# Performance work log

Measured on AMD Instinct MI355X. Metric: run time of the kernel, lower is better.

## Reference

```python
import jax, jax.numpy as jnp
import numpy as np

DEPTH = 2
DIM = 192
HEADS = 6
MLP_RATIO = 4

def _layernorm(x, g, b):
    mu = jnp.mean(x, -1, keepdims=True)
    var = jnp.var(x, -1, keepdims=True)
    return (x - mu) * jax.lax.rsqrt(var + 1e-5) * g + b

def _scanline_order(pos, w):
    # default space-filling curve of space_filling_cluster: horizontal scanlines
    # with alternating direction in each row (boustrophedon order)
    ix = jnp.floor(pos[..., 0]).astype(jnp.int32)
    iy = jnp.floor(pos[..., 1]).astype(jnp.int32)
    key = iy * w + jnp.where(iy % 2 == 1, w - 1 - ix, ix)
    order_idx = jnp.argsort(key, axis=1)      # rank -> token idx (b, n)
    inv_idx = jnp.argsort(order_idx, axis=1)  # token idx -> rank (b, n)
    return order_idx, inv_idx

def setup_inputs():
    key = jax.random.key(0)
    ks = jax.random.split(key, 8)
    b, h, w, m = 4, 128, 128, 64
    n = h * w
    d = DIM
    dff = MLP_RATIO * d
    s = 0.02
    x = jax.random.normal(ks[0], (b, n, d), jnp.float32)
    # token positions: the full h x w grid, randomly permuted per batch element
    ys, xs = jnp.meshgrid(jnp.arange(h), jnp.arange(w), indexing='ij')
    grid = jnp.stack([xs.reshape(-1), ys.reshape(-1)], -1).astype(jnp.float32)
    perm = jax.vmap(lambda kk: jax.random.permutation(kk, n))(jax.random.split(ks[1], b))
    pos = grid[perm]  # (b, n, 2)
    return {
        'x': x, 'pos': pos,
        'ln1_g': jnp.ones((DEPTH, d)), 'ln1_b': jnp.zeros((DEPTH, d)),
        'w_qkv': jax.random.normal(ks[2], (DEPTH, d, 3 * d), jnp.float32) * s,
        'b_qkv': jnp.zeros((DEPTH, 3 * d)),
        'w_proj': jax.random.normal(ks[3], (DEPTH, d, d), jnp.float32) * s,
        'b_proj': jnp.zeros((DEPTH, d)),
        'ln2_g': jnp.ones((DEPTH, d)), 'ln2_b': jnp.zeros((DEPTH, d)),
        'w_fc1': jax.random.normal(ks[4], (DEPTH, d, dff), jnp.float32) * s,
        'b_fc1': jnp.zeros((DEPTH, dff)),
        'w_fc2': jax.random.normal(ks[5], (DEPTH, dff, d), jnp.float32) * s,
        'b_fc2': jnp.zeros((DEPTH, d)),
        'h': h, 'w': w, 'm': m,
    }

def reference(x, pos, ln1_g, ln1_b, w_qkv, b_qkv, w_proj, b_proj,
              ln2_g, ln2_b, w_fc1, b_fc1, w_fc2, b_fc2, h, w, m):
    b, n, d = x.shape
    dh = d // HEADS
    scale = dh ** -0.5
    kc = n // m  # number of clusters (n chosen divisible by m -> all-ones cluster_mask)
    # clustering is computed under no_grad in the original -> stop_gradient
    order_idx, inv_idx = _scanline_order(jax.lax.stop_gradient(pos), w)
    for i in range(DEPTH):
        # --- cluster attention ---
        xn = _layernorm(x, ln1_g[i], ln1_b[i])
        qkv = xn @ w_qkv[i] + b_qkv[i]                                  # (b, n, 3d)
        qkv = jnp.take_along_axis(qkv, order_idx[..., None], axis=1)    # gather into curve order
        qkv = qkv.reshape(b, kc, m, 3, HEADS, dh)
        q = jnp.transpose(qkv[:, :, :, 0], (0, 1, 3, 2, 4))             # (b, kc, H, m, dh)
        kk = jnp.transpose(qkv[:, :, :, 1], (0, 1, 3, 2, 4))
        v = jnp.transpose(qkv[:, :, :, 2], (0, 1, 3, 2, 4))
        att = jax.nn.softmax(jnp.einsum('bkhqd,bkhpd->bkhqp', q, kk) * scale, axis=-1)
        o = jnp.einsum('bkhqp,bkhpd->bkhqd', att, v)
        o = jnp.transpose(o, (0, 1, 3, 2, 4)).reshape(b, n, d)
        o = jnp.take_along_axis(o, inv_idx[..., None], axis=1)          # scatter back to token order
        x = x + o @ w_proj[i] + b_proj[i]
        # --- MLP ---
        yn = _layernorm(x, ln2_g[i], ln2_b[i])
        x = x + jax.nn.gelu(yn @ w_fc1[i] + b_fc1[i]) @ w_fc2[i] + b_fc2[i]
    return x
```

## Files before the change

### kernel.cpp

```cpp
#include <hip/hip_runtime.h>
#include <hip/hip_bf16.h>

typedef __hip_bfloat16 bf16;
typedef __attribute__((ext_vector_type(8))) short short8;
typedef __attribute__((ext_vector_type(4))) short s16x4;
typedef __attribute__((ext_vector_type(4))) float f32x4;

#define B_   4
#define N_   16384
#define D_   192
#define H6   6
#define DH   32
#define MCL  64
#define KC   256
#define DFF  768
#define GW   128
#define MTOK (B_ * N_)
#define XST  196

__device__ __forceinline__ bf16 f2b(float x) { return __float2bfloat16(x); }
__device__ __forceinline__ short f2bbits(float x) {
    bf16 h = __float2bfloat16(x); return *(short*)&h;
}

__global__ void zero_out_kernel(float* __restrict__ out, size_t n) {
    size_t i = blockIdx.x * (size_t)blockDim.x + threadIdx.x;
    if (i < n) out[i] = 0.f;
}

__global__ void build_idx(const float* __restrict__ pos, int* __restrict__ order) {
    int tid = blockIdx.x * blockDim.x + threadIdx.x;
    if (tid >= B_ * N_) return;
    int b = tid / N_;
    int ix = (int)floorf(pos[(size_t)tid * 2 + 0]);
    int iy = (int)floorf(pos[(size_t)tid * 2 + 1]);
    int key = iy * GW + ((iy & 1) ? (GW - 1 - ix) : ix);
    key = (int)(((unsigned)key) & (N_ - 1));
    order[(size_t)b * N_ + key] = tid % N_;
}

__global__ void wprep_all(const float* __restrict__ wq, const float* __restrict__ wp,
                          const float* __restrict__ wf1, const float* __restrict__ wf2,
                          bf16* __restrict__ out) {
    int tid = blockIdx.x * blockDim.x + threadIdx.x;
    if (tid >= 2 * 442368) return;
    int l = tid / 442368, r = tid % 442368;
    const float* src; bf16* dst; int K, Nn, e;
    if (r < 110592)      { src = wq  + (size_t)l * 110592; dst = out + (size_t)l * 442368;          K = 192; Nn = 576; e = r; }
    else if (r < 147456) { src = wp  + (size_t)l * 36864;  dst = out + (size_t)l * 442368 + 110592; K = 192; Nn = 192; e = r - 110592; }
    else if (r < 294912) { src = wf1 + (size_t)l * 147456; dst = out + (size_t)l * 442368 + 147456; K = 192; Nn = 768; e = r - 147456; }
    else                 { src = wf2 + (size_t)l * 147456; dst = out + (size_t)l * 442368 + 294912; K = 768; Nn = 192; e = r - 294912; }
    int k = e / Nn, n = e % Nn;
    int idx = ((n >> 4) * (K >> 5) + (k >> 5)) * 512 + (((k >> 3) & 3) * 16 + (n & 15)) * 8 + (k & 7);
    dst[idx] = f2b(src[e]);
}

template<bool GELU>
__global__ __launch_bounds__(256, 4) void gemm_lnk192(
    const float* __restrict__ Ain, const float* __restrict__ lng, const float* __restrict__ lnb,
    const bf16* __restrict__ Wf, const float* __restrict__ bias,
    bf16* __restrict__ Cout, int Nn) {
    __shared__ short Asl[4 * 6 * 512];
    int tid = threadIdx.x;
    int bm = blockIdx.x;
    int w = tid >> 6, lane = tid & 63;
    {
        int r = tid >> 2, qq = tid & 3;
        const float* xr = Ain + ((size_t)(bm * 64) + r) * 192 + qq * 48;
        float4 va[12];
        float s = 0.f, ss = 0.f;
        #pragma unroll
        for (int j = 0; j < 12; j++) {
            va[j] = ((const float4*)xr)[j];
            s  += va[j].x + va[j].y + va[j].z + va[j].w;
            ss += va[j].x * va[j].x + va[j].y * va[j].y + va[j].z * va[j].z + va[j].w * va[j].w;
        }
        s  += __shfl_xor(s, 1);  s  += __shfl_xor(s, 2);
        ss += __shfl_xor(ss, 1); ss += __shfl_xor(ss, 2);
        float mean = s * (1.f / 192.f);
        float var  = ss * (1.f / 192.f) - mean * mean;
        float rs   = rsqrtf(var + 1e-5f);
        const float4* gg = (const float4*)(lng + qq * 48);
        const float4* bb = (const float4*)(lnb + qq * 48);
        #pragma unroll
        for (int j = 0; j < 6; j++) {
            float4 g0 = gg[2 * j], g1 = gg[2 * j + 1], b0 = bb[2 * j], b1 = bb[2 * j + 1];
            float4 x0 = va[2 * j], x1 = va[2 * j + 1];
            short8 o;
            o[0] = f2bbits((x0.x - mean) * rs * g0.x + b0.x);
            o[1] = f2bbits((x0.y - mean) * rs * g0.y + b0.y);
            o[2] = f2bbits((x0.z - mean) * rs * g0.z + b0.z);
            o[3] = f2bbits((x0.w - mean) * rs * g0.w + b0.w);
            o[4] = f2bbits((x1.x - mean) * rs * g1.x + b1.x);
            o[5] = f2bbits((x1.y - mean) * rs * g1.y + b1.y);
            o[6] = f2bbits((x1.z - mean) * rs * g1.z + b1.z);
            o[7] = f2bbits((x1.w - mean) * rs * g1.w + b1.w);
            int k0 = qq * 48 + j * 8;
            int kt = k0 >> 5, qd = (k0 >> 3) & 3;
            *(short8*)&Asl[((r >> 4) * 6 + kt) * 512 + (qd * 16 + (r & 15)) * 8] = o;
        }
    }
    __syncthreads();
    short8 af[6];
    #pragma unroll
    for (int kt = 0; kt < 6; kt++)
        af[kt] = *(short8*)&Asl[(w * 6 + kt) * 512 + lane * 8];
    int quad = lane >> 4, l16 = lane & 15;
    int ntiles = Nn >> 4;
    for (int nt = 0; nt < ntiles; nt++) {
        const short* bp = (const short*)Wf + ((size_t)nt * 6) * 512 + lane * 8;
        f32x4 acc = {};
        #pragma unroll
        for (int kt = 0; kt < 6; kt++) {
            short8 b = *(const short8*)(bp + kt * 512);
            acc = __builtin_amdgcn_mfma_f32_16x16x32_bf16(af[kt], b, acc, 0, 0, 0);
        }
        int col = nt * 16 + l16;
        float bv = bias[col];
        int row0 = bm * 64 + w * 16 + quad * 4;
        #pragma unroll
        for (int rr = 0; rr < 4; rr++) {
            float v = acc[rr] + bv;
            if (GELU) {
                float inner = 0.7978845608028654f * (v + 0.044715f * v * v * v);
                inner = fminf(fmaxf(inner, -12.f), 12.f);
                float e = __expf(2.f * inner);
                v = 0.5f * v * (1.f + (e - 1.f) / (e + 1.f));
            }
            Cout[(size_t)(row0 + rr) * Nn + col] = f2b(v);
        }
    }
}

__global__ __launch_bounds__(256) void pm_fused(
    const bf16* __restrict__ Anob,
    const bf16* __restrict__ Wpf, const float* __restrict__ bp_,
    const float* __restrict__ Rsrc,
    const float* __restrict__ lng, const float* __restrict__ lnb,
    const bf16* __restrict__ W1f, const float* __restrict__ b1,
    const bf16* __restrict__ W2f, const float* __restrict__ b2,
    float* __restrict__ Rdst) {
    __shared__ float Xl[64 * XST];
    __shared__ short Bsl[4 * 6 * 512];
    short* Asl = (short*)Xl;
    int tid = threadIdx.x;
    int bm = blockIdx.x;
    int w = tid >> 6, lane = tid & 63;
    int quad = lane >> 4, l16 = lane & 15;
    {
        int r = tid >> 2, qq = tid & 3;
        const short* ar = (const short*)Anob + ((size_t)(bm * 64) + r) * 192 + qq * 48;
        #pragma unroll
        for (int j = 0; j < 6; j++) {
            short8 v = *(const short8*)(ar + j * 8);
            int k0 = qq * 48 + j * 8;
            int kt = k0 >> 5, qd = (k0 >> 3) & 3;
            *(short8*)&Asl[((r >> 4) * 6 + kt) * 512 + (qd * 16 + (r & 15)) * 8] = v;
        }
    }
    __syncthreads();
    short8 afp[6];
    #pragma unroll
    for (int kt = 0; kt < 6; kt++)
        afp[kt] = *(short8*)&Asl[(w * 6 + kt) * 512 + lane * 8];
    f32x4 acc[12];
    #pragma unroll
    for (int nt = 0; nt < 12; nt++) {
        const short* bp = (const short*)Wpf + ((size_t)nt * 6) * 512 + lane * 8;
        f32x4 a = {};
        #pragma unroll
        for (int kt = 0; kt < 6; kt++) {
            short8 b = *(const short8*)(bp + kt * 512);
            a = __builtin_amdgcn_mfma_f32_16x16x32_bf16(afp[kt], b, a, 0, 0, 0);
        }
        acc[nt] = a;
    }
    __syncthreads();
    #pragma unroll
    for (int nt = 0; nt < 12; nt++) {
        int col = nt * 16 + l16;
        float bv = bp_[col];
        int lr0 = w * 16 + quad * 4;
        #pragma unroll
        for (int rr = 0; rr < 4; rr++) {
            float rv = Rsrc[(size_t)(bm * 64 + lr0 + rr) * 192 + col];
            Xl[(lr0 + rr) * XST + col] = acc[nt][rr] + bv + rv;
        }
    }
    __syncthreads();
    {
        int r = tid >> 2, qq = tid & 3;
        const float* xr = &Xl[r * XST + qq * 48];
        float4 va[12];
        float s = 0.f, ss = 0.f;
        #pragma unroll
        for (int j = 0; j < 12; j++) {
            va[j] = ((const float4*)xr)[j];
            s  += va[j].x + va[j].y + va[j].z + va[j].w;
            ss += va[j].x * va[j].x + va[j].y * va[j].y + va[j].z * va[j].z + va[j].w * va[j].w;
        }
        s  += __shfl_xor(s, 1);  s  += __shfl_xor(s, 2);
        ss += __shfl_xor(ss, 1); ss += __shfl_xor(ss, 2);
        float mean = s * (1.f / 192.f);
        float var  = ss * (1.f / 192.f) - mean * mean;
        float rs   = rsqrtf(var + 1e-5f);
        const float4* gg = (const float4*)(lng + qq * 48);
        const float4* bb = (const float4*)(lnb + qq * 48);
        #pragma unroll
        for (int j = 0; j < 6; j++) {
            float4 g0 = gg[2 * j], g1 = gg[2 * j + 1], b0 = bb[2 * j], b1v = bb[2 * j + 1];
            float4 x0 = va[2 * j], x1 = va[2 * j + 1];
            short8 o;
            o[0] = f2bbits((x0.x - mean) * rs * g0.x + b0.x);
            o[1] = f2bbits((x0.y - mean) * rs * g0.y + b0.y);
            o[2] = f2bbits((x0.z - mean) * rs * g0.z + b0.z);
            o[3] = f2bbits((x0.w - mean) * rs * g0.w + b0.w);
            o[4] = f2bbits((x1.x - mean) * rs * g1.x + b1v.x);
            o[5] = f2bbits((x1.y - mean) * rs * g1.y + b1v.y);
            o[6] = f2bbits((x1.z - mean) * rs * g1.z + b1v.z);
            o[7] = f2bbits((x1.w - mean) * rs * g1.w + b1v.w);
            int k0 = qq * 48 + j * 8;
            int kt = k0 >> 5, qd = (k0 >> 3) & 3;
            *(short8*)&Bsl[((r >> 4) * 6 + kt) * 512 + (qd * 16 + (r & 15)) * 8] = o;
        }
    }
    __syncthreads();
    short8 af[4][6];
    #pragma unroll
    for (int mt = 0; mt < 4; mt++)
        #pragma unroll
        for (int kt = 0; kt < 6; kt++)
            af[mt][kt] = *(short8*)&Bsl[(mt * 6 + kt) * 512 + lane * 8];
    f32x4 acc2[3][4] = {};
    for (int qtr = 0; qtr < 4; qtr++) {
        __syncthreads();
        #pragma unroll
        for (int j = 0; j < 3; j++) {
            int nth = w * 3 + j;
            int ntg = qtr * 12 + nth;
            const short* bp = (const short*)W1f + ((size_t)ntg * 6) * 512 + lane * 8;
            short8 bfr[6];
            #pragma unroll
            for (int kt = 0; kt < 6; kt++) bfr[kt] = *(const short8*)(bp + kt * 512);
            #pragma unroll
            for (int mt = 0; mt < 4; mt++) {
                f32x4 a = {};
                #pragma unroll
                for (int kt = 0; kt < 6; kt++)
                    a = __builtin_amdgcn_mfma_f32_16x16x32_bf16(bfr[kt], af[mt][kt], a, 0, 0, 0);
                int colb = ntg * 16 + quad * 4;
                s16x4 o;
                #pragma unroll
                for (int rr = 0; rr < 4; rr++) {
                    float u = a[rr] + b1[colb + rr];
                    float inner = 0.7978845608028654f * (u + 0.044715f * u * u * u);
                    inner = fminf(fmaxf(inner, -12.f), 12.f);
                    float e = __expf(2.f * inner);
                    o[rr] = f2bbits(0.5f * u * (1.f + (e - 1.f) / (e + 1.f)));
                }
                *(s16x4*)&Bsl[(mt * 6 + (nth >> 1)) * 512
                              + (((nth & 1) * 2 + (quad >> 1)) * 16 + l16) * 8 + (quad & 1) * 4] = o;
            }
        }
        __syncthreads();
        #pragma unroll
        for (int kt = 0; kt < 6; kt++) {
            short8 afh[4];
            #pragma unroll
            for (int mt = 0; mt < 4; mt++)
                afh[mt] = *(short8*)&Bsl[(mt * 6 + kt) * 512 + lane * 8];
            #pragma unroll
            for (int j = 0; j < 3; j++) {
                int nt = w * 3 + j;
                const short* bp = (const short*)W2f + ((size_t)nt * 24 + qtr * 6 + kt) * 512 + lane * 8;
                short8 b = *(const short8*)bp;
                #pragma unroll
                for (int mt = 0; mt < 4; mt++)
                    acc2[j][mt] = __builtin_amdgcn_mfma_f32_16x16x32_bf16(afh[mt], b, acc2[j][mt], 0, 0, 0);
            }
        }
    }
    #pragma unroll
    for (int j = 0; j < 3; j++) {
        int col = (w * 3 + j) * 16 + l16;
        float bv = b2[col];
        #pragma unroll
        for (int mt = 0; mt < 4; mt++) {
            int lr0 = mt * 16 + quad * 4;
            #pragma unroll
            for (int rr = 0; rr < 4; rr++) {
                size_t idx = (size_t)(bm * 64 + lr0 + rr) * 192 + col;
                Rdst[idx] = acc2[j][mt][rr] + bv + Xl[(lr0 + rr) * XST + col];
            }
        }
    }
}

#define PST 72
#define VST 72
#define OST 40
__global__ __launch_bounds__(64) void attn_mfma(const bf16* __restrict__ qkv,
                                                const int* __restrict__ order,
                                                bf16* __restrict__ outb) {
    __shared__ short vT[32 * VST];
    __shared__ short Pl[64 * PST];
    const float scale = 0.17677669529663687f;
    int h = blockIdx.x, c = blockIdx.y, b = blockIdx.z;
    int lane = threadIdx.x;
    int l16 = lane & 15, quad = lane >> 4;
    int t = (int)(((unsigned)order[(size_t)b * N_ + c * MCL + lane]) & (N_ - 1));
    const short* qb = (const short*)qkv + (size_t)b * N_ * 576;
    {
        const short* vp = qb + (size_t)t * 576 + 384 + h * 32;
        short8 v[4];
        #pragma unroll
        for (int i = 0; i < 4; i++) v[i] = *(const short8*)(vp + i * 8);
        #pragma unroll
        for (int i = 0; i < 4; i++)
            #pragma unroll
            for (int e = 0; e < 8; e++)
                vT[(i * 8 + e) * VST + lane] = v[i][e];
    }
    short8 aq[4], bk[4];
    #pragma unroll
    for (int i = 0; i < 4; i++) {
        int tr = __shfl(t, i * 16 + l16);
        const short* rp = qb + (size_t)tr * 576 + h * 32 + quad * 8;
        aq[i] = *(const short8*)rp;
        bk[i] = *(const short8*)(rp + 192);
    }
    f32x4 S[4][4];
    #pragma unroll
    for (int mt = 0; mt < 4; mt++)
        #pragma unroll
        for (int nt = 0; nt < 4; nt++) {
            f32x4 z = {};
            S[mt][nt] = __builtin_amdgcn_mfma_f32_16x16x32_bf16(aq[mt], bk[nt], z, 0, 0, 0);
        }
    __syncthreads();
    #pragma unroll
    for (int mt = 0; mt < 4; mt++)
        #pragma unroll
        for (int r = 0; r < 4; r++) {
            float e0, e1, e2, e3, s;
            float v0 = S[mt][0][r] * scale, v1 = S[mt][1][r] * scale;
            float v2 = S[mt][2][r] * scale, v3 = S[mt][3][r] * scale;
            e0 = __expf(fminf(fmaxf(v0, -30.f), 30.f));
            e1 = __expf(fminf(fmaxf(v1, -30.f), 30.f));
            e2 = __expf(fminf(fmaxf(v2, -30.f), 30.f));
            e3 = __expf(fminf(fmaxf(v3, -30.f), 30.f));
            s = e0 + e1 + e2 + e3;
            s += __shfl_xor(s, 1); s += __shfl_xor(s, 2);
            s += __shfl_xor(s, 4); s += __shfl_xor(s, 8);
            float inv = 1.f / s;
            int row = mt * 16 + quad * 4 + r;
            Pl[row * PST +  0 + l16] = f2bbits(e0 * inv);
            Pl[row * PST + 16 + l16] = f2bbits(e1 * inv);
            Pl[row * PST + 32 + l16] = f2bbits(e2 * inv);
            Pl[row * PST + 48 + l16] = f2bbits(e3 * inv);
        }
    __syncthreads();
    short8 ap[4][2], bv[2][2];
    #pragma unroll
    for (int mt = 0; mt < 4; mt++)
        #pragma unroll
        for (int kt = 0; kt < 2; kt++)
            ap[mt][kt] = *(const short8*)&Pl[(mt * 16 + l16) * PST + kt * 32 + quad * 8];
    #pragma unroll
    for (int nt = 0; nt < 2; nt++)
        #pragma unroll
        for (int kt = 0; kt < 2; kt++)
            bv[nt][kt] = *(const short8*)&vT[(nt * 16 + l16) * VST + kt * 32 + quad * 8];
    f32x4 O[4][2] = {};
    #pragma unroll
    for (int mt = 0; mt < 4; mt++)
        #pragma unroll
        for (int nt = 0; nt < 2; nt++)
            #pragma unroll
            for (int kt = 0; kt < 2; kt++)
                O[mt][nt] = __builtin_amdgcn_mfma_f32_16x16x32_bf16(ap[mt][kt], bv[nt][kt], O[mt][nt], 0, 0, 0);
    __syncthreads();
    short* Ol = Pl;
    #pragma unroll
    for (int mt = 0; mt < 4; mt++) {
        int row = mt * 16 + quad * 4;
        #pragma unroll
        for (int nt = 0; nt < 2; nt++)
            #pragma unroll
            for (int rr = 0; rr < 4; rr++)
                Ol[(row + rr) * OST + nt * 16 + l16] = f2bbits(O[mt][nt][rr]);
    }
    __syncthreads();
    short* op = (short*)outb + ((size_t)b * N_ + t) * 192 + h * 32;
    #pragma unroll
    for (int j = 0; j < 4; j++)
        *(short8*)(op + j * 8) = *(const short8*)&Ol[lane * OST + j * 8];
}

extern "C" void kernel_launch(void* const* d_in, const int* in_sizes, int n_in,
                              void* d_out, int out_size, void* d_ws, size_t ws_size,
                              hipStream_t stream) {
    const float* x_in   = (const float*)d_in[0];
    const float* pos    = (const float*)d_in[1];
    const float* ln1_g  = (const float*)d_in[2];
    const float* ln1_b  = (const float*)d_in[3];
    const float* w_qkv  = (const float*)d_in[4];
    const float* b_qkv  = (const float*)d_in[5];
    const float* w_proj = (const float*)d_in[6];
    const float* b_proj = (const float*)d_in[7];
    const float* ln2_g  = (const float*)d_in[8];
    const float* ln2_b  = (const float*)d_in[9];
    const float* w_fc1  = (const float*)d_in[10];
    const float* b_fc1  = (const float*)d_in[11];
    const float* w_fc2  = (const float*)d_in[12];
    const float* b_fc2  = (const float*)d_in[13];

    size_t sz_x     = (size_t)MTOK * D_ * 4;
    size_t sz_xnob  = (size_t)MTOK * D_ * 2;
    size_t sz_cbuf  = (size_t)MTOK * DFF * 2;
    size_t sz_order = (size_t)B_ * N_ * 4;
    size_t sz_wbuf  = (size_t)2 * 442368 * 2;
    size_t need = sz_x + sz_xnob + sz_cbuf + sz_order + sz_wbuf;
    if (ws_size < need) {
        zero_out_kernel<<<(out_size + 255) / 256, 256, 0, stream>>>((float*)d_out, (size_t)out_size);
        return;
    }
    char* ws = (char*)d_ws;
    float* x_f32 = (float*)ws;  ws += sz_x;
    bf16*  xnob  = (bf16*)ws;   ws += sz_xnob;
    bf16*  cbuf  = (bf16*)ws;   ws += sz_cbuf;
    int*   order = (int*)ws;    ws += sz_order;
    bf16*  wbuf  = (bf16*)ws;   ws += sz_wbuf;

    bf16* wq[2]; bf16* wp[2]; bf16* wf1[2]; bf16* wf2[2];
    for (int l = 0; l < 2; ++l) {
        bf16* p = wbuf + (size_t)l * 442368;
        wq[l]  = p;
        wp[l]  = p + 110592;
        wf1[l] = p + 147456;
        wf2[l] = p + 294912;
    }
    wprep_all<<<(2 * 442368 + 255) / 256, 256, 0, stream>>>(w_qkv, w_proj, w_fc1, w_fc2, wbuf);
    build_idx<<<(B_ * N_ + 255) / 256, 256, 0, stream>>>(pos, order);

    for (int l = 0; l < 2; ++l) {
        const float* xsrc = (l == 0) ? x_in : x_f32;
        float* rdst = (l == 1) ? (float*)d_out : x_f32;
        gemm_lnk192<false><<<MTOK / 64, 256, 0, stream>>>(
            xsrc, ln1_g + l * D_, ln1_b + l * D_, wq[l], b_qkv + l * 576, cbuf, 576);
        attn_mfma<<<dim3(H6, KC, B_), 64, 0, stream>>>(cbuf, order, xnob);
        pm_fused<<<MTOK / 64, 256, 0, stream>>>(
            xnob, wp[l], b_proj + l * 192, xsrc,
            ln2_g + l * D_, ln2_b + l * D_,
            wf1[l], b_fc1 + l * 768, wf2[l], b_fc2 + l * 192,
            rdst);
    }
}
```

Baseline: 510.5 us.

## Fuse LayerNorm, QKV projection and cluster attention into one kernel

Replaces the separate LN+QKV GEMM kernel and the per-head attention kernel with one kernel that runs per cluster and batch element. The kernel gathers the cluster's token rows in curve order, applies LayerNorm, and computes Q, K and V into shared memory with one wave per head. Each wave then runs softmax attention on its own head and writes the output back to token order. This removes the full qkv intermediate buffer and its global write and reread. In exchange it needs a large shared-memory footprint and 384-thread blocks, which may limit how many blocks fit on each CU.

New measurement: 440.3 us. 1.16x faster.

```diff
diff --git a/kernel.cpp b/kernel.cpp
--- a/kernel.cpp
+++ b/kernel.cpp
@@ -17,6 +17,8 @@
 #define GW   128
 #define MTOK (B_ * N_)
 #define XST  196
+#define PST  72
+#define OST  40
 
 __device__ __forceinline__ bf16 f2b(float x) { return __float2bfloat16(x); }
 __device__ __forceinline__ short f2bbits(float x) {
@@ -55,18 +57,26 @@
     dst[idx] = f2b(src[e]);
 }
 
-template<bool GELU>
-__global__ __launch_bounds__(256, 4) void gemm_lnk192(
-    const float* __restrict__ Ain, const float* __restrict__ lng, const float* __restrict__ lnb,
-    const bf16* __restrict__ Wf, const float* __restrict__ bias,
-    bf16* __restrict__ Cout, int Nn) {
+__global__ __launch_bounds__(384) void qa_fused(
+    const float* __restrict__ xsrc, const int* __restrict__ order,
+    const float* __restrict__ lng, const float* __restrict__ lnb,
+    const bf16* __restrict__ Wqf, const float* __restrict__ bq,
+    bf16* __restrict__ outb) {
     __shared__ short Asl[4 * 6 * 512];
+    __shared__ short Qf[4 * 6 * 512];
+    __shared__ short Kf[4 * 6 * 512];
+    __shared__ short Vf[6 * 4 * 512];
+    __shared__ short Pm[6 * 64 * PST];
+    const float scale = 0.17677669529663687f;
+    int c = blockIdx.x, b = blockIdx.y;
     int tid = threadIdx.x;
-    int bm = blockIdx.x;
     int w = tid >> 6, lane = tid & 63;
-    {
+    int quad = lane >> 4, l16 = lane & 15;
+    int t = (int)(((unsigned)order[(size_t)b * N_ + c * MCL + lane]) & (N_ - 1));
+    if (tid < 256) {
         int r = tid >> 2, qq = tid & 3;
-        const float* xr = Ain + ((size_t)(bm * 64) + r) * 192 + qq * 48;
+        int tr = (int)(((unsigned)order[(size_t)b * N_ + c * MCL + r]) & (N_ - 1));
+        const float* xr = xsrc + ((size_t)b * N_ + tr) * 192 + qq * 48;
         float4 va[12];
         float s = 0.f, ss = 0.f;
         #pragma unroll
@@ -84,52 +94,142 @@
         const float4* bb = (const float4*)(lnb + qq * 48);
         #pragma unroll
         for (int j = 0; j < 6; j++) {
-            float4 g0 = gg[2 * j], g1 = gg[2 * j + 1], b0 = bb[2 * j], b1 = bb[2 * j + 1];
+            float4 g0 = gg[2 * j], g1 = gg[2 * j + 1], b0 = bb[2 * j], b1v = bb[2 * j + 1];
             float4 x0 = va[2 * j], x1 = va[2 * j + 1];
             short8 o;
             o[0] = f2bbits((x0.x - mean) * rs * g0.x + b0.x);
             o[1] = f2bbits((x0.y - mean) * rs * g0.y + b0.y);
             o[2] = f2bbits((x0.z - mean) * rs * g0.z + b0.z);
             o[3] = f2bbits((x0.w - mean) * rs * g0.w + b0.w);
-            o[4] = f2bbits((x1.x - mean) * rs * g1.x + b1.x);
-            o[5] = f2bbits((x1.y - mean) * rs * g1.y + b1.y);
-            o[6] = f2bbits((x1.z - mean) * rs * g1.z + b1.z);
-            o[7] = f2bbits((x1.w - mean) * rs * g1.w + b1.w);
+            o[4] = f2bbits((x1.x - mean) * rs * g1.x + b1v.x);
+            o[5] = f2bbits((x1.y - mean) * rs * g1.y + b1v.y);
+            o[6] = f2bbits((x1.z - mean) * rs * g1.z + b1v.z);
+            o[7] = f2bbits((x1.w - mean) * rs * g1.w + b1v.w);
             int k0 = qq * 48 + j * 8;
             int kt = k0 >> 5, qd = (k0 >> 3) & 3;
             *(short8*)&Asl[((r >> 4) * 6 + kt) * 512 + (qd * 16 + (r & 15)) * 8] = o;
         }
     }
     __syncthreads();
-    short8 af[6];
-    #pragma unroll
-    for (int kt = 0; kt < 6; kt++)
-        af[kt] = *(short8*)&Asl[(w * 6 + kt) * 512 + lane * 8];
-    int quad = lane >> 4, l16 = lane & 15;
-    int ntiles = Nn >> 4;
-    for (int nt = 0; nt < ntiles; nt++) {
-        const short* bp = (const short*)Wf + ((size_t)nt * 6) * 512 + lane * 8;
-        f32x4 acc = {};
-        #pragma unroll
-        for (int kt = 0; kt < 6; kt++) {
-            short8 b = *(const short8*)(bp + kt * 512);
-            acc = __builtin_amdgcn_mfma_f32_16x16x32_bf16(af[kt], b, acc, 0, 0, 0);
-        }
-        int col = nt * 16 + l16;
-        float bv = bias[col];
-        int row0 = bm * 64 + w * 16 + quad * 4;
-        #pragma unroll
-        for (int rr = 0; rr < 4; rr++) {
-            float v = acc[rr] + bv;
-            if (GELU) {
-                float inner = 0.7978845608028654f * (v + 0.044715f * v * v * v);
-                inner = fminf(fmaxf(inner, -12.f), 12.f);
-                float e = __expf(2.f * inner);
-                v = 0.5f * v * (1.f + (e - 1.f) / (e + 1.f));
-            }
-            Cout[(size_t)(row0 + rr) * Nn + col] = f2b(v);
-        }
-    }
+    short8 af[4][6];
+    #pragma unroll
+    for (int mt = 0; mt < 4; mt++)
+        #pragma unroll
+        for (int kt = 0; kt < 6; kt++)
+            af[mt][kt] = *(short8*)&Asl[(mt * 6 + kt) * 512 + lane * 8];
+    #pragma unroll
+    for (int s = 0; s < 4; s++) {
+        int isK = s >> 1, q = s & 1;
+        int nt = isK * 12 + 2 * w + q;
+        const short* bp = (const short*)Wqf + ((size_t)nt * 6) * 512 + lane * 8;
+        short8 bfr[6];
+        #pragma unroll
+        for (int kt = 0; kt < 6; kt++) bfr[kt] = *(const short8*)(bp + kt * 512);
+        float4 bvq = *(const float4*)(bq + nt * 16 + quad * 4);
+        short* dstb = isK ? Kf : Qf;
+        #pragma unroll
+        for (int mt = 0; mt < 4; mt++) {
+            f32x4 a = {};
+            #pragma unroll
+            for (int kt = 0; kt < 6; kt++)
+                a = __builtin_amdgcn_mfma_f32_16x16x32_bf16(bfr[kt], af[mt][kt], a, 0, 0, 0);
+            s16x4 o;
+            o[0] = f2bbits(a[0] + bvq.x); o[1] = f2bbits(a[1] + bvq.y);
+            o[2] = f2bbits(a[2] + bvq.z); o[3] = f2bbits(a[3] + bvq.w);
+            *(s16x4*)&dstb[(mt * 6 + w) * 512
+                           + ((q * 2 + (quad >> 1)) * 16 + l16) * 8 + (quad & 1) * 4] = o;
+        }
+    }
+    #pragma unroll
+    for (int q = 0; q < 2; q++) {
+        int nt = 24 + 2 * w + q;
+        const short* bp = (const short*)Wqf + ((size_t)nt * 6) * 512 + lane * 8;
+        short8 bfr[6];
+        #pragma unroll
+        for (int kt = 0; kt < 6; kt++) bfr[kt] = *(const short8*)(bp + kt * 512);
+        float bvv = bq[nt * 16 + l16];
+        #pragma unroll
+        for (int mt = 0; mt < 4; mt++) {
+            f32x4 a = {};
+            #pragma unroll
+            for (int kt = 0; kt < 6; kt++)
+                a = __builtin_amdgcn_mfma_f32_16x16x32_bf16(af[mt][kt], bfr[kt], a, 0, 0, 0);
+            s16x4 o;
+            #pragma unroll
+            for (int rr = 0; rr < 4; rr++) o[rr] = f2bbits(a[rr] + bvv);
+            *(s16x4*)&Vf[((w * 2 + q) * 2 + (mt >> 1)) * 512
+                         + (((mt & 1) * 2 + (quad >> 1)) * 16 + l16) * 8 + (quad & 1) * 4] = o;
+        }
+    }
+    short8 aq[4], bk[4];
+    #pragma unroll
+    for (int i = 0; i < 4; i++) {
+        aq[i] = *(short8*)&Qf[(i * 6 + w) * 512 + lane * 8];
+        bk[i] = *(short8*)&Kf[(i * 6 + w) * 512 + lane * 8];
+    }
+    f32x4 S[4][4];
+    #pragma unroll
+    for (int mt = 0; mt < 4; mt++)
+        #pragma unroll
+        for (int nt = 0; nt < 4; nt++) {
+            f32x4 z = {};
+            S[mt][nt] = __builtin_amdgcn_mfma_f32_16x16x32_bf16(aq[mt], bk[nt], z, 0, 0, 0);
+        }
+    short* Pl = Pm + w * 64 * PST;
+    #pragma unroll
+    for (int mt = 0; mt < 4; mt++)
+        #pragma unroll
+        for (int r = 0; r < 4; r++) {
+            float e0, e1, e2, e3, s;
+            float v0 = S[mt][0][r] * scale, v1 = S[mt][1][r] * scale;
+            float v2 = S[mt][2][r] * scale, v3 = S[mt][3][r] * scale;
+            e0 = __expf(fminf(fmaxf(v0, -30.f), 30.f));
+            e1 = __expf(fminf(fmaxf(v1, -30.f), 30.f));
+            e2 = __expf(fminf(fmaxf(v2, -30.f), 30.f));
+            e3 = __expf(fminf(fmaxf(v3, -30.f), 30.f));
+            s = e0 + e1 + e2 + e3;
+            s += __shfl_xor(s, 1); s += __shfl_xor(s, 2);
+            s += __shfl_xor(s, 4); s += __shfl_xor(s, 8);
+            float inv = 1.f / s;
+            int row = mt * 16 + quad * 4 + r;
+            Pl[row * PST +  0 + l16] = f2bbits(e0 * inv);
+            Pl[row * PST + 16 + l16] = f2bbits(e1 * inv);
+            Pl[row * PST + 32 + l16] = f2bbits(e2 * inv);
+            Pl[row * PST + 48 + l16] = f2bbits(e3 * inv);
+        }
+    short8 ap[4][2], bv[2][2];
+    #pragma unroll
+    for (int mt = 0; mt < 4; mt++)
+        #pragma unroll
+        for (int kt = 0; kt < 2; kt++)
+            ap[mt][kt] = *(const short8*)&Pl[(mt * 16 + l16) * PST + kt * 32 + quad * 8];
+    #pragma unroll
+    for (int nt = 0; nt < 2; nt++)
+        #pragma unroll
+        for (int kt = 0; kt < 2; kt++)
+            bv[nt][kt] = *(const short8*)&Vf[((w * 2 + nt) * 2 + kt) * 512 + lane * 8];
+    f32x4 O[4][2] = {};
+    #pragma unroll
+    for (int mt = 0; mt < 4; mt++)
+        #pragma unroll
+        for (int nt = 0; nt < 2; nt++)
+            #pragma unroll
+            for (int kt = 0; kt < 2; kt++)
+                O[mt][nt] = __builtin_amdgcn_mfma_f32_16x16x32_bf16(ap[mt][kt], bv[nt][kt], O[mt][nt], 0, 0, 0);
+    short* Ol = Pl;
+    #pragma unroll
+    for (int mt = 0; mt < 4; mt++) {
+        int row = mt * 16 + quad * 4;
+        #pragma unroll
+        for (int nt = 0; nt < 2; nt++)
+            #pragma unroll
+            for (int rr = 0; rr < 4; rr++)
+                Ol[(row + rr) * OST + nt * 16 + l16] = f2bbits(O[mt][nt][rr]);
+    }
+    short* op = (short*)outb + ((size_t)b * N_ + t) * 192 + w * 32;
+    #pragma unroll
+    for (int j = 0; j < 4; j++)
+        *(short8*)(op + j * 8) = *(const short8*)&Ol[lane * OST + j * 8];
 }
 
 __global__ __launch_bounds__(256) void pm_fused(
@@ -296,107 +396,6 @@
     }
 }
 
-#define PST 72
-#define VST 72
-#define OST 40
-__global__ __launch_bounds__(64) void attn_mfma(const bf16* __restrict__ qkv,
-                                                const int* __restrict__ order,
-                                                bf16* __restrict__ outb) {
-    __shared__ short vT[32 * VST];
-    __shared__ short Pl[64 * PST];
-    const float scale = 0.17677669529663687f;
-    int h = blockIdx.x, c = blockIdx.y, b = blockIdx.z;
-    int lane = threadIdx.x;
-    int l16 = lane & 15, quad = lane >> 4;
-    int t = (int)(((unsigned)order[(size_t)b * N_ + c * MCL + lane]) & (N_ - 1));
-    const short* qb = (const short*)qkv + (size_t)b * N_ * 576;
-    {
-        const short* vp = qb + (size_t)t * 576 + 384 + h * 32;
-        short8 v[4];
-        #pragma unroll
-        for (int i = 0; i < 4; i++) v[i] = *(const short8*)(vp + i * 8);
-        #pragma unroll
-        for (int i = 0; i < 4; i++)
-            #pragma unroll
-            for (int e = 0; e < 8; e++)
-                vT[(i * 8 + e) * VST + lane] = v[i][e];
-    }
-    short8 aq[4], bk[4];
-    #pragma unroll
-    for (int i = 0; i < 4; i++) {
-        int tr = __shfl(t, i * 16 + l16);
-        const short* rp = qb + (size_t)tr * 576 + h * 32 + quad * 8;
-        aq[i] = *(const short8*)rp;
-        bk[i] = *(const short8*)(rp + 192);
-    }
-    f32x4 S[4][4];
-    #pragma unroll
-    for (int mt = 0; mt < 4; mt++)
-        #pragma unroll
-        for (int nt = 0; nt < 4; nt++) {
-            f32x4 z = {};
-            S[mt][nt] = __builtin_amdgcn_mfma_f32_16x16x32_bf16(aq[mt], bk[nt], z, 0, 0, 0);
-        }
-    __syncthreads();
-    #pragma unroll
-    for (int mt = 0; mt < 4; mt++)
-        #pragma unroll
-        for (int r = 0; r < 4; r++) {
-            float e0, e1, e2, e3, s;
-            float v0 = S[mt][0][r] * scale, v1 = S[mt][1][r] * scale;
-            float v2 = S[mt][2][r] * scale, v3 = S[mt][3][r] * scale;
-            e0 = __expf(fminf(fmaxf(v0, -30.f), 30.f));
-            e1 = __expf(fminf(fmaxf(v1, -30.f), 30.f));
-            e2 = __expf(fminf(fmaxf(v2, -30.f), 30.f));
-            e3 = __expf(fminf(fmaxf(v3, -30.f), 30.f));
-            s = e0 + e1 + e2 + e3;
-            s += __shfl_xor(s, 1); s += __shfl_xor(s, 2);
-            s += __shfl_xor(s, 4); s += __shfl_xor(s, 8);
-            float inv = 1.f / s;
-            int row = mt * 16 + quad * 4 + r;
-            Pl[row * PST +  0 + l16] = f2bbits(e0 * inv);
-            Pl[row * PST + 16 + l16] = f2bbits(e1 * inv);
-            Pl[row * PST + 32 + l16] = f2bbits(e2 * inv);
-            Pl[row * PST + 48 + l16] = f2bbits(e3 * inv);
-        }
-    __syncthreads();
-    short8 ap[4][2], bv[2][2];
-    #pragma unroll
-    for (int mt = 0; mt < 4; mt++)
-        #pragma unroll
-        for (int kt = 0; kt < 2; kt++)
-            ap[mt][kt] = *(const short8*)&Pl[(mt * 16 + l16) * PST + kt * 32 + quad * 8];
-    #pragma unroll
-    for (int nt = 0; nt < 2; nt++)
-        #pragma unroll
-        for (int kt = 0; kt < 2; kt++)
-            bv[nt][kt] = *(const short8*)&vT[(nt * 16 + l16) * VST + kt * 32 + quad * 8];
-    f32x4 O[4][2] = {};
-    #pragma unroll
-    for (int mt = 0; mt < 4; mt++)
-        #pragma unroll
-        for (int nt = 0; nt < 2; nt++)
-            #pragma unroll
-            for (int kt = 0; kt < 2; kt++)
-                O[mt][nt] = __builtin_amdgcn_mfma_f32_16x16x32_bf16(ap[mt][kt], bv[nt][kt], O[mt][nt], 0, 0, 0);
-    __syncthreads();
-    short* Ol = Pl;
-    #pragma unroll
-    for (int mt = 0; mt < 4; mt++) {
-        int row = mt * 16 + quad * 4;
-        #pragma unroll
-        for (int nt = 0; nt < 2; nt++)
-            #pragma unroll
-            for (int rr = 0; rr < 4; rr++)
-                Ol[(row + rr) * OST + nt * 16 + l16] = f2bbits(O[mt][nt][rr]);
-    }
-    __syncthreads();
-    short* op = (short*)outb + ((size_t)b * N_ + t) * 192 + h * 32;
-    #pragma unroll
-    for (int j = 0; j < 4; j++)
-        *(short8*)(op + j * 8) = *(const short8*)&Ol[lane * OST + j * 8];
-}
-
 extern "C" void kernel_launch(void* const* d_in, const int* in_sizes, int n_in,
                               void* d_out, int out_size, void* d_ws, size_t ws_size,
                               hipStream_t stream) {
@@ -417,10 +416,9 @@
 
     size_t sz_x     = (size_t)MTOK * D_ * 4;
     size_t sz_xnob  = (size_t)MTOK * D_ * 2;
-    size_t sz_cbuf  = (size_t)MTOK * DFF * 2;
     size_t sz_order = (size_t)B_ * N_ * 4;
     size_t sz_wbuf  = (size_t)2 * 442368 * 2;
-    size_t need = sz_x + sz_xnob + sz_cbuf + sz_order + sz_wbuf;
+    size_t need = sz_x + sz_xnob + sz_order + sz_wbuf;
     if (ws_size < need) {
         zero_out_kernel<<<(out_size + 255) / 256, 256, 0, stream>>>((float*)d_out, (size_t)out_size);
         return;
@@ -428,7 +426,6 @@
     char* ws = (char*)d_ws;
     float* x_f32 = (float*)ws;  ws += sz_x;
     bf16*  xnob  = (bf16*)ws;   ws += sz_xnob;
-    bf16*  cbuf  = (bf16*)ws;   ws += sz_cbuf;
     int*   order = (int*)ws;    ws += sz_order;
     bf16*  wbuf  = (bf16*)ws;   ws += sz_wbuf;
 
@@ -446,9 +443,9 @@
     for (int l = 0; l < 2; ++l) {
         const float* xsrc = (l == 0) ? x_in : x_f32;
         float* rdst = (l == 1) ? (float*)d_out : x_f32;
-        gemm_lnk192<false><<<MTOK / 64, 256, 0, stream>>>(
-            xsrc, ln1_g + l * D_, ln1_b + l * D_, wq[l], b_qkv + l * 576, cbuf, 576);
-        attn_mfma<<<dim3(H6, KC, B_), 64, 0, stream>>>(cbuf, order, xnob);
+        qa_fused<<<dim3(KC, B_), 384, 0, stream>>>(
+            xsrc, order, ln1_g + l * D_, ln1_b + l * D_,
+            wq[l], b_qkv + l * 576, xnob);
         pm_fused<<<MTOK / 64, 256, 0, stream>>>(
             xnob, wp[l], b_proj + l * 192, xsrc,
             ln2_g + l * D_, ln2_b + l * D_,
```
